# Kernel optimization log

Measured on AMD Instinct MI355X. Metric: run time of the kernel, lower is better.

Reference implementation:

```python
import jax, jax.numpy as jnp
import numpy as np

B, C, L = 16, 256, 2048

def setup_inputs() -> dict:
    key = jax.random.key(0)
    k1, k2, k3, k4 = jax.random.split(key, 4)
    return {
        "proj_query": jax.random.normal(k1, (B, C, L), dtype=jnp.float32),
        "proj_key": jax.random.normal(k2, (B, C, L), dtype=jnp.float32),
        "proj_val": jax.random.normal(k3, (B, C, L), dtype=jnp.float32),
        "padding_mask": jax.random.uniform(k4, (B, 1, L), dtype=jnp.float32),
    }

def reference(proj_query, proj_key, proj_val, padding_mask):
    c = proj_query.shape[1]
    # energy[b,l,m] = sum_c Q[b,c,l] * K[b,c,m]  -> (B, L, L)
    energy = jnp.einsum("bcl,bcm->blm", proj_query, proj_key) / jnp.sqrt(jnp.float32(c))
    # log-additive padding mask (the tril mask in the source is dead code, never applied)
    logits = energy + jnp.log(padding_mask + 1e-9)
    attention = jax.nn.softmax(logits, axis=-1)
    # post-softmax multiplicative mask
    attention = attention * padding_mask
    # out[b,c,l] = sum_m V[b,c,m] * attention[b,l,m]  -> (B, C, L)
    out = jnp.einsum("bcm,blm->bcl", proj_val, attention)
    return out
```

## Files before the change

### kernel.cpp

```cpp
#include <hip/hip_runtime.h>
#include <hip/hip_bf16.h>

#define B_ 16
#define C_ 256
#define L_ 2048
#define KVB 32
#define NT (L_ / KVB)

typedef __attribute__((ext_vector_type(8))) short bf16x8;
typedef __attribute__((ext_vector_type(4))) unsigned u32x4;
typedef __attribute__((ext_vector_type(16))) float f32x16;

#define CEXP 0.09016844005556021f

__device__ __forceinline__ short f2bf_rne(float f) {
    union { float f; unsigned u; } x; x.f = f;
    unsigned r = x.u + 0x7fffu + ((x.u >> 16) & 1u);
    return (short)(r >> 16);
}

__device__ __forceinline__ unsigned pack2(float lo, float hi) {
    return (unsigned)(unsigned short)f2bf_rne(lo)
         | ((unsigned)(unsigned short)f2bf_rne(hi) << 16);
}

__device__ __forceinline__ void gld_lds16(const void* g, void* l) {
    __builtin_amdgcn_global_load_lds(
        (const __attribute__((address_space(1))) void*)g,
        (__attribute__((address_space(3))) void*)l, 16, 0, 0);
}

__global__ __launch_bounds__(256) void prepass_kernel(
        const float* __restrict__ Kin, const float* __restrict__ Vin,
        const float* __restrict__ mask,
        short* __restrict__ Kt, short* __restrict__ Vb) {
    const int bid = blockIdx.x;
    const int t = threadIdx.x;
    if (bid < 512) {
        __shared__ unsigned short tile[64 * 256];
        const int b  = bid >> 5;
        const int l0 = (bid & 31) * 64;
        #pragma unroll
        for (int iter = 0; iter < 8; ++iter) {
            int l  = t & 63;
            int ck = (t >> 6) + 4 * iter;
            const float* src = Kin + ((size_t)(b * C_ + 8 * ck)) * L_ + l0 + l;
            unsigned pk[4];
            #pragma unroll
            for (int jj = 0; jj < 4; ++jj) {
                float f0 = src[(size_t)(2 * jj) * L_];
                float f1 = src[(size_t)(2 * jj + 1) * L_];
                pk[jj] = pack2(f0, f1);
            }
            uint4 o = {pk[0], pk[1], pk[2], pk[3]};
            *(uint4*)(tile + l * 256 + ((ck ^ (l & 31)) << 3)) = o;
        }
        __syncthreads();
        #pragma unroll
        for (int iter = 0; iter < 8; ++iter) {
            int li = iter * 8 + (t >> 5);
            int ck = t & 31;
            uint4 val = *(const uint4*)(tile + li * 256 + ((ck ^ (li & 31)) << 3));
            *(uint4*)(Kt + ((size_t)(b * L_ + l0 + li)) * C_ + ck * 8) = val;
        }
    } else {
        size_t e = ((size_t)(bid - 512) * 256 + t) * 8;
        int b = (int)(e >> 19);
        int m = (int)(e & (L_ - 1));
        const float4 v0 = *(const float4*)(Vin + e);
        const float4 v1 = *(const float4*)(Vin + e + 4);
        const float* mp = mask + ((size_t)b << 11) + m;
        const float4 m0 = *(const float4*)mp;
        const float4 m1 = *(const float4*)(mp + 4);
        uint4 o;
        o.x = pack2(v0.x * m0.x, v0.y * m0.y);
        o.y = pack2(v0.z * m0.z, v0.w * m0.w);
        o.z = pack2(v1.x * m1.x, v1.y * m1.y);
        o.w = pack2(v1.z * m1.z, v1.w * m1.w);
        *(uint4*)(Vb + e) = o;
    }
}

__device__ __forceinline__ void stage_K(const short* __restrict__ Ksrc,
                                        short* Ks, int m0, int t) {
    #pragma unroll
    for (int rr = 0; rr < 4; ++rr) {
        int G = rr * 256 + t;
        int m = G >> 5, p = G & 31;
        gld_lds16(Ksrc + ((size_t)(m0 + m) << 8) + ((p ^ m) << 3), Ks + G * 8);
    }
}

__device__ __forceinline__ void stage_V(const short* __restrict__ Vsrc,
                                        short* Vs, int m0, int t) {
    #pragma unroll
    for (int rr = 0; rr < 4; ++rr) {
        int G = rr * 256 + t;
        int c = G >> 2, p = G & 3;
        gld_lds16(Vsrc + (size_t)c * L_ + m0 + ((p ^ ((c >> 1) & 3)) << 3), Vs + G * 8);
    }
}

#define TILE_BODY(KS, VS, M0)                                                               \
  {                                                                                         \
    const short* Krow = (KS) + ln * 256;                                                    \
    bf16x8 kf[16];                                                                          \
    _Pragma("unroll")                                                                       \
    for (int ki = 0; ki < 16; ++ki)                                                         \
      kf[ki] = *(const bf16x8*)(Krow + (((2 * ki + h) ^ ln) << 3));                         \
    float4 mk[4];                                                                           \
    _Pragma("unroll")                                                                       \
    for (int s = 0; s < 4; ++s) mk[s] = *(const float4*)(mrow + (M0) + 8 * s + 4 * h);      \
    f32x16 s0 = z16, s1 = z16;                                                              \
    _Pragma("unroll")                                                                       \
    for (int ki = 0; ki < 8; ++ki)                                                          \
      s0 = __builtin_amdgcn_mfma_f32_32x32x16_bf16(kf[ki], qf[ki], s0, 0, 0, 0);            \
    _Pragma("unroll")                                                                       \
    for (int ki = 8; ki < 16; ++ki)                                                         \
      s1 = __builtin_amdgcn_mfma_f32_32x32x16_bf16(kf[ki], qf[ki], s1, 0, 0, 0);            \
    unsigned wds[8];                                                                        \
    _Pragma("unroll")                                                                       \
    for (int u = 0; u < 8; ++u) {                                                           \
      const int ra = 2 * u, rb = 2 * u + 1;                                                 \
      float fa = (mk[ra >> 2][ra & 3] + 1e-9f) * exp2f(s0[ra] + s1[ra]);                    \
      float fb = (mk[rb >> 2][rb & 3] + 1e-9f) * exp2f(s0[rb] + s1[rb]);                    \
      dn += fa + fb;                                                                        \
      wds[u] = pack2(fa, fb);                                                               \
    }                                                                                       \
    unsigned e0 = __shfl_xor(h ? wds[0] : wds[2], 32, 64);                                  \
    unsigned e1 = __shfl_xor(h ? wds[1] : wds[3], 32, 64);                                  \
    unsigned e2 = __shfl_xor(h ? wds[4] : wds[6], 32, 64);                                  \
    unsigned e3 = __shfl_xor(h ? wds[5] : wds[7], 32, 64);                                  \
    u32x4 b1u = { h ? e0 : wds[0], h ? e1 : wds[1], h ? wds[2] : e0, h ? wds[3] : e1 };     \
    u32x4 b2u = { h ? e2 : wds[4], h ? e3 : wds[5], h ? wds[6] : e2, h ? wds[7] : e3 };     \
    bf16x8 b1 = __builtin_bit_cast(bf16x8, b1u);                                            \
    bf16x8 b2 = __builtin_bit_cast(bf16x8, b2u);                                            \
    const int vsw = (ln >> 1) & 3;                                                          \
    _Pragma("unroll")                                                                       \
    for (int ct = 0; ct < 8; ++ct) {                                                        \
      const short* Vrow = (VS) + (32 * ct + ln) * 32;                                       \
      bf16x8 av1 = *(const bf16x8*)(Vrow + ((h ^ vsw) << 3));                               \
      bf16x8 av2 = *(const bf16x8*)(Vrow + (((2 + h) ^ vsw) << 3));                         \
      Oacc[ct] = __builtin_amdgcn_mfma_f32_32x32x16_bf16(av1, b1, Oacc[ct], 0, 0, 0);       \
      Oacc[ct] = __builtin_amdgcn_mfma_f32_32x32x16_bf16(av2, b2, Oacc[ct], 0, 0, 0);       \
    }                                                                                       \
  }

__global__ __launch_bounds__(256, 1) void attn_main(
        const float* __restrict__ Qin,
        const short* __restrict__ Kt,
        const short* __restrict__ Vb,
        const float* __restrict__ mask,
        float* __restrict__ out) {
    __shared__ __align__(16) char smem[65536];
    short* KsB0 = (short*)smem;
    short* KsB1 = (short*)(smem + 16384);
    short* VsB0 = (short*)(smem + 32768);
    short* VsB1 = (short*)(smem + 49152);

    const int t = threadIdx.x;
    const int w = t >> 6, lane = t & 63;
    const int ln = lane & 31, h = lane >> 5;

    const int b  = blockIdx.x & 15;
    const int l0 = (blockIdx.x >> 4) * 128;
    const int lw = l0 + 32 * w;

    const short* Ksrc = Kt + (size_t)b * (L_ * C_);
    const short* Vsrc = Vb + (size_t)b * (C_ * L_);
    const float* mrow = mask + (size_t)b * L_;

    stage_K(Ksrc, KsB0, 0, t);
    stage_V(Vsrc, VsB0, 0, t);

    bf16x8 qf[16];
    {
        const float* Qb = Qin + (size_t)b * (C_ * L_) + (lw + ln);
        #pragma unroll
        for (int ki = 0; ki < 16; ++ki) {
            bf16x8 v;
            #pragma unroll
            for (int j = 0; j < 8; ++j) {
                float f = Qb[(size_t)(16 * ki + 8 * h + j) * L_];
                v[j] = f2bf_rne(f * CEXP);
            }
            qf[ki] = v;
        }
    }

    const f32x16 z16 = {0.f,0.f,0.f,0.f,0.f,0.f,0.f,0.f,0.f,0.f,0.f,0.f,0.f,0.f,0.f,0.f};
    f32x16 Oacc[8];
    #pragma unroll
    for (int ct = 0; ct < 8; ++ct) Oacc[ct] = z16;
    float dn = 0.f;

    __syncthreads();

    #pragma unroll 1
    for (int it2 = 0; it2 < NT / 2; ++it2) {
        const int m0a = it2 * (2 * KVB);
        const int m0b = m0a + KVB;

        stage_K(Ksrc, KsB1, m0b, t);
        stage_V(Vsrc, VsB1, m0b, t);
        TILE_BODY(KsB0, VsB0, m0a)
        __syncthreads();

        if (m0b + KVB < L_) {
            stage_K(Ksrc, KsB0, m0b + KVB, t);
            stage_V(Vsrc, VsB0, m0b + KVB, t);
        }
        TILE_BODY(KsB1, VsB1, m0b)
        __syncthreads();
    }

    dn += __shfl_xor(dn, 32, 64);
    const float rden = 1.0f / dn;

    float* ob = out + (size_t)b * (C_ * L_) + lw + ln;
    #pragma unroll
    for (int ct = 0; ct < 8; ++ct)
        #pragma unroll
        for (int r = 0; r < 16; ++r) {
            int c = 32 * ct + (r & 3) + 8 * (r >> 2) + 4 * h;
            ob[(size_t)c * L_] = Oacc[ct][r] * rden;
        }
}

extern "C" void kernel_launch(void* const* d_in, const int* in_sizes, int n_in,
                              void* d_out, int out_size, void* d_ws, size_t ws_size,
                              hipStream_t stream) {
    const float* Q    = (const float*)d_in[0];
    const float* K    = (const float*)d_in[1];
    const float* V    = (const float*)d_in[2];
    const float* mask = (const float*)d_in[3];
    float* out = (float*)d_out;

    short* Kt = (short*)d_ws;
    short* Vb = Kt + (size_t)B_ * L_ * C_;

    prepass_kernel<<<4608, 256, 0, stream>>>(K, V, mask, Kt, Vb);
    attn_main<<<256, 256, 0, stream>>>(Q, Kt, Vb, mask, out);
}
```

Before: 235.1 us.

## Split KV range across two blocks per query tile and combine partials

The attention kernel now divides the key/value sequence into two halves handled by separate workgroups, which doubles the grid from 256 to 512 blocks so it can fill more CUs on the device. Each half writes unnormalized output partials and denominators to workspace, and a new combine kernel sums them and normalizes. Launch bounds are relaxed to allow two blocks per CU. In exchange it adds an extra kernel launch plus a large fp32 partial write and read-back of about 64 MB, and it only takes effect if the workspace is large enough.

```diff
diff --git a/kernel.cpp b/kernel.cpp
--- a/kernel.cpp
+++ b/kernel.cpp
@@ -146,12 +146,15 @@
     }                                                                                       \
   }
 
-__global__ __launch_bounds__(256, 1) void attn_main(
+__global__ __launch_bounds__(256, 2) void attn_main(
         const float* __restrict__ Qin,
         const short* __restrict__ Kt,
         const short* __restrict__ Vb,
         const float* __restrict__ mask,
-        float* __restrict__ out) {
+        float* __restrict__ out,
+        float* __restrict__ Opart,
+        float* __restrict__ Dnpart,
+        const int split) {
     __shared__ __align__(16) char smem[65536];
     short* KsB0 = (short*)smem;
     short* KsB1 = (short*)(smem + 16384);
@@ -162,16 +165,23 @@
     const int w = t >> 6, lane = t & 63;
     const int ln = lane & 31, h = lane >> 5;
 
-    const int b  = blockIdx.x & 15;
-    const int l0 = (blockIdx.x >> 4) * 128;
+    int inner, half;
+    if (split) { half = blockIdx.x >> 8; inner = blockIdx.x & 255; }
+    else       { half = 0;               inner = blockIdx.x; }
+    const int b  = inner & 15;
+    const int l0 = (inner >> 4) * 128;
     const int lw = l0 + 32 * w;
+
+    const int m_base = half * (L_ / 2);
+    const int n_it2  = split ? (NT / 4) : (NT / 2);
+    const int m_end  = m_base + n_it2 * 2 * KVB;
 
     const short* Ksrc = Kt + (size_t)b * (L_ * C_);
     const short* Vsrc = Vb + (size_t)b * (C_ * L_);
     const float* mrow = mask + (size_t)b * L_;
 
-    stage_K(Ksrc, KsB0, 0, t);
-    stage_V(Vsrc, VsB0, 0, t);
+    stage_K(Ksrc, KsB0, m_base, t);
+    stage_V(Vsrc, VsB0, m_base, t);
 
     bf16x8 qf[16];
     {
@@ -197,8 +207,8 @@
     __syncthreads();
 
     #pragma unroll 1
-    for (int it2 = 0; it2 < NT / 2; ++it2) {
-        const int m0a = it2 * (2 * KVB);
+    for (int it2 = 0; it2 < n_it2; ++it2) {
+        const int m0a = m_base + it2 * (2 * KVB);
         const int m0b = m0a + KVB;
 
         stage_K(Ksrc, KsB1, m0b, t);
@@ -206,7 +216,7 @@
         TILE_BODY(KsB0, VsB0, m0a)
         __syncthreads();
 
-        if (m0b + KVB < L_) {
+        if (m0b + KVB < m_end) {
             stage_K(Ksrc, KsB0, m0b + KVB, t);
             stage_V(Vsrc, VsB0, m0b + KVB, t);
         }
@@ -215,16 +225,47 @@
     }
 
     dn += __shfl_xor(dn, 32, 64);
-    const float rden = 1.0f / dn;
-
-    float* ob = out + (size_t)b * (C_ * L_) + lw + ln;
-    #pragma unroll
-    for (int ct = 0; ct < 8; ++ct)
-        #pragma unroll
-        for (int r = 0; r < 16; ++r) {
-            int c = 32 * ct + (r & 3) + 8 * (r >> 2) + 4 * h;
-            ob[(size_t)c * L_] = Oacc[ct][r] * rden;
-        }
+
+    if (split) {
+        if (h == 0) Dnpart[(size_t)half * (B_ * L_) + b * L_ + lw + ln] = dn;
+        float* op = Opart + (size_t)half * ((size_t)B_ * C_ * L_)
+                  + (size_t)b * (C_ * L_) + lw + ln;
+        #pragma unroll
+        for (int ct = 0; ct < 8; ++ct)
+            #pragma unroll
+            for (int r = 0; r < 16; ++r) {
+                int c = 32 * ct + (r & 3) + 8 * (r >> 2) + 4 * h;
+                op[(size_t)c * L_] = Oacc[ct][r];
+            }
+    } else {
+        const float rden = 1.0f / dn;
+        float* ob = out + (size_t)b * (C_ * L_) + lw + ln;
+        #pragma unroll
+        for (int ct = 0; ct < 8; ++ct)
+            #pragma unroll
+            for (int r = 0; r < 16; ++r) {
+                int c = 32 * ct + (r & 3) + 8 * (r >> 2) + 4 * h;
+                ob[(size_t)c * L_] = Oacc[ct][r] * rden;
+            }
+    }
+}
+
+__global__ __launch_bounds__(256) void combine_kernel(
+        const float* __restrict__ Opart, const float* __restrict__ Dnpart,
+        float* __restrict__ out) {
+    size_t e = ((size_t)blockIdx.x * 256 + threadIdx.x) * 4;
+    int b = (int)(e >> 19);
+    int l = (int)(e & (L_ - 1));
+    float4 o0 = *(const float4*)(Opart + e);
+    float4 o1 = *(const float4*)(Opart + (size_t)B_ * C_ * L_ + e);
+    float4 d0 = *(const float4*)(Dnpart + b * L_ + l);
+    float4 d1 = *(const float4*)(Dnpart + B_ * L_ + b * L_ + l);
+    float4 r;
+    r.x = (o0.x + o1.x) / (d0.x + d1.x);
+    r.y = (o0.y + o1.y) / (d0.y + d1.y);
+    r.z = (o0.z + o1.z) / (d0.z + d1.z);
+    r.w = (o0.w + o1.w) / (d0.w + d1.w);
+    *(float4*)(out + e) = r;
 }
 
 extern "C" void kernel_launch(void* const* d_in, const int* in_sizes, int n_in,
@@ -236,9 +277,20 @@
     const float* mask = (const float*)d_in[3];
     float* out = (float*)d_out;
 
+    const size_t kv_bytes = (size_t)2 * B_ * L_ * C_ * sizeof(short);
+    const size_t op_bytes = (size_t)2 * B_ * C_ * L_ * sizeof(float);
+    const size_t dn_bytes = (size_t)2 * B_ * L_ * sizeof(float);
     short* Kt = (short*)d_ws;
     short* Vb = Kt + (size_t)B_ * L_ * C_;
+    float* Op = (float*)((char*)d_ws + kv_bytes);
+    float* Dn = (float*)((char*)d_ws + kv_bytes + op_bytes);
+    const bool use_split = ws_size >= kv_bytes + op_bytes + dn_bytes;
 
     prepass_kernel<<<4608, 256, 0, stream>>>(K, V, mask, Kt, Vb);
-    attn_main<<<256, 256, 0, stream>>>(Q, Kt, Vb, mask, out);
-}
+    if (use_split) {
+        attn_main<<<512, 256, 0, stream>>>(Q, Kt, Vb, mask, out, Op, Dn, 1);
+        combine_kernel<<<8192, 256, 0, stream>>>(Op, Dn, out);
+    } else {
+        attn_main<<<256, 256, 0, stream>>>(Q, Kt, Vb, mask, out, nullptr, nullptr, 0);
+    }
+}
```

Measured after the change: 410.3 us. +74.5%, slower.
